# Kernel optimization log

Measured on AMD Instinct MI355X. Metric: run time of the kernel, lower is better.

Reference implementation:

```python
import jax, jax.numpy as jnp
import numpy as np

BEAMS, TEMP, DEPTH, K = 8, 0.4, 3, 3   # beams, router temperature, max_depth, n_experts
EPS, NEG = 1e-5, -1e9

def _conv(x, w, b):
    y = jax.lax.conv_general_dilated(x, w, (1, 1), 'VALID',
                                     dimension_numbers=('NCHW', 'OIHW', 'NCHW'))
    return y + b[None, :, None, None]

def _bn(x, g, b, m, v):
    inv = g * jax.lax.rsqrt(v + EPS)
    return x * inv[None, :, None, None] + (b - m * inv)[None, :, None, None]

def _pool(x):  # AvgPool2d(2)
    return jax.lax.reduce_window(x, 0.0, jax.lax.add, (1, 1, 2, 2), (1, 1, 2, 2), 'VALID') * 0.25

def _fwd(x, conv1_w, conv1_b, bn1_g, bn1_b, bn1_m, bn1_v,
         conv2_w, conv2_b, bn2_g, bn2_b, bn2_m, bn2_v,
         conv3_w, conv3_b, bn3_g, bn3_b, bn3_m, bn3_v,
         Wxh, Whh, bh, Who, bo, emb, Wexp, bexp, Wout, bout):
    B = x.shape[0]
    h = _pool(jax.nn.relu(_bn(_conv(x, conv1_w, conv1_b), bn1_g, bn1_b, bn1_m, bn1_v)))
    h = _pool(jax.nn.relu(_bn(_conv(h, conv2_w, conv2_b), bn2_g, bn2_b, bn2_m, bn2_v)))
    h = _pool(jax.nn.relu(_bn(_conv(h, conv3_w, conv3_b), bn3_g, bn3_b, bn3_m, bn3_v)))
    feat = h.reshape(B, -1)                                  # (B,128)
    # --- beam search over length-3 op sequences with RNN router ---
    hr = jnp.broadcast_to(feat[:, None, :], (B, BEAMS, 128))  # router hidden, (B,beams,128)
    scores = jnp.full((B, BEAMS), NEG, dtype=x.dtype).at[:, 0].set(0.0)
    ops_seq = []
    for _ in range(DEPTH):
        logits = jnp.einsum('bkd,do->bko', hr, Who) + bo      # (B,beams,3)
        logp = jax.nn.log_softmax(logits / TEMP, axis=-1)
        total = (scores[..., None] + logp).reshape(B, BEAMS * K)
        scores, idx = jax.lax.top_k(total, BEAMS)             # (B,beams)
        beam_idx, op = idx // K, idx % K
        hr = jnp.take_along_axis(hr, beam_idx[..., None], axis=1)
        hr = jnp.tanh(hr @ Whh + emb[op] @ Wxh + bh)
        ops_seq = [jnp.take_along_axis(o, beam_idx, axis=1) for o in ops_seq]
        ops_seq.append(op)
    # --- top-1 routed expert chain (grouped gather-GEMM instead of per-sample loop) ---
    hs = jnp.broadcast_to(feat[:, None, :], (B, BEAMS, 128)).reshape(B * BEAMS, 128)
    for op in ops_seq:
        o = op.reshape(B * BEAMS)
        hs = jax.nn.relu(jnp.einsum('nd,ndk->nk', hs, Wexp[o]) + bexp[o])
    return jax.nn.log_softmax(hs @ Wout + bout, axis=1)      # (B*beams,10)

def setup_inputs() -> dict:
    key = jax.random.key(0)
    ks = jax.random.split(key, 20)
    n = lambda i, shape, s: jax.random.normal(ks[i], shape, jnp.float32) * s
    d = {
        'x': jax.random.normal(ks[0], (512, 1, 32, 32), jnp.float32),
        'conv1_w': n(1, (32, 1, 3, 3), 0.2),  'conv1_b': n(2, (32,), 0.02),
        'bn1_g': jnp.ones((32,), jnp.float32), 'bn1_b': jnp.zeros((32,), jnp.float32),
        'bn1_m': jnp.zeros((32,), jnp.float32), 'bn1_v': jnp.ones((32,), jnp.float32),
        'conv2_w': n(3, (32, 32, 3, 3), 0.06), 'conv2_b': n(4, (32,), 0.02),
        'bn2_g': jnp.ones((32,), jnp.float32), 'bn2_b': jnp.zeros((32,), jnp.float32),
        'bn2_m': jnp.zeros((32,), jnp.float32), 'bn2_v': jnp.ones((32,), jnp.float32),
        'conv3_w': n(5, (32, 32, 3, 3), 0.06), 'conv3_b': n(6, (32,), 0.02),
        'bn3_g': jnp.ones((32,), jnp.float32), 'bn3_b': jnp.zeros((32,), jnp.float32),
        'bn3_m': jnp.zeros((32,), jnp.float32), 'bn3_v': jnp.ones((32,), jnp.float32),
        'Wxh': n(7, (128, 128), 0.09), 'Whh': n(8, (128, 128), 0.09), 'bh': n(9, (128,), 0.02),
        'Who': n(10, (128, 3), 0.09), 'bo': n(11, (3,), 0.02), 'emb': n(12, (3, 128), 0.5),
        'Wexp': n(13, (3, 128, 128), 0.09), 'bexp': n(14, (3, 128), 0.02),
        'Wout': n(15, (128, 10), 0.09), 'bout': n(16, (10,), 0.02),
    }
    return d

def reference(x, conv1_w, conv1_b, bn1_g, bn1_b, bn1_m, bn1_v,
              conv2_w, conv2_b, bn2_g, bn2_b, bn2_m, bn2_v,
              conv3_w, conv3_b, bn3_g, bn3_b, bn3_m, bn3_v,
              Wxh, Whh, bh, Who, bo, emb, Wexp, bexp, Wout, bout):
    return _fwd(x, conv1_w, conv1_b, bn1_g, bn1_b, bn1_m, bn1_v,
                conv2_w, conv2_b, bn2_g, bn2_b, bn2_m, bn2_v,
                conv3_w, conv3_b, bn3_g, bn3_b, bn3_m, bn3_v,
                Wxh, Whh, bh, Who, bo, emb, Wexp, bexp, Wout, bout)
```

## Files before the change

### kernel.cpp

```cpp
#include <hip/hip_runtime.h>
#include <math.h>

__global__ __launch_bounds__(512) void conv1_k(
    const float* __restrict__ x, const float* __restrict__ w,
    const float* __restrict__ cb, const float* __restrict__ bg,
    const float* __restrict__ bb, const float* __restrict__ bm,
    const float* __restrict__ bv, float* __restrict__ h1)
{
    __shared__ float img[32 * 33];
    __shared__ float ws_[288];
    __shared__ float scale[32], bias2[32];
    const int b = blockIdx.x, tid = threadIdx.x;
    for (int i = tid; i < 1024; i += 512) {
        const int y = i >> 5, xx = i & 31;
        img[y * 33 + xx] = x[b * 1024 + i];
    }
    if (tid < 288) ws_[tid] = w[tid];
    if (tid < 32) {
        float inv = bg[tid] / sqrtf(bv[tid] + 1e-5f);
        scale[tid] = inv;
        bias2[tid] = (cb[tid] - bm[tid]) * inv + bb[tid];
    }
    __syncthreads();

    const int co = tid >> 4, py = tid & 15;
    if (py < 15) {
        float acc0[30], acc1[30];
        #pragma unroll
        for (int i = 0; i < 30; ++i) { acc0[i] = 0.f; acc1[i] = 0.f; }
        const float* w9 = &ws_[co * 9];
        #pragma unroll
        for (int ir = 0; ir < 4; ++ir) {
            const int y = 2 * py + ir;
            float wk0 = 0.f, wk1 = 0.f, wk2 = 0.f, wl0 = 0.f, wl1 = 0.f, wl2 = 0.f;
            if (ir <= 2) { wk0 = w9[ir * 3 + 0]; wk1 = w9[ir * 3 + 1]; wk2 = w9[ir * 3 + 2]; }
            if (ir >= 1) { wl0 = w9[(ir - 1) * 3 + 0]; wl1 = w9[(ir - 1) * 3 + 1]; wl2 = w9[(ir - 1) * 3 + 2]; }
            #pragma unroll
            for (int xx = 0; xx < 32; ++xx) {
                const float rv = img[y * 33 + xx];
                if (ir <= 2) {
                    if (xx <= 29) acc0[xx] += rv * wk0;
                    if (xx >= 1 && xx <= 30) acc0[xx - 1] += rv * wk1;
                    if (xx >= 2) acc0[xx - 2] += rv * wk2;
                }
                if (ir >= 1) {
                    if (xx <= 29) acc1[xx] += rv * wl0;
                    if (xx >= 1 && xx <= 30) acc1[xx - 1] += rv * wl1;
                    if (xx >= 2) acc1[xx - 2] += rv * wl2;
                }
            }
        }
        const float sc = scale[co], bs = bias2[co];
        #pragma unroll
        for (int px = 0; px < 15; ++px) {
            const float v = fmaxf(acc0[2 * px] * sc + bs, 0.f)
                          + fmaxf(acc0[2 * px + 1] * sc + bs, 0.f)
                          + fmaxf(acc1[2 * px] * sc + bs, 0.f)
                          + fmaxf(acc1[2 * px + 1] * sc + bs, 0.f);
            h1[b * 7200 + co * 225 + py * 15 + px] = v * 0.25f;
        }
    }
}

__global__ __launch_bounds__(384) void conv2_k(
    const float* __restrict__ h1, const float* __restrict__ w,
    const float* __restrict__ cb, const float* __restrict__ bg,
    const float* __restrict__ bb, const float* __restrict__ bm,
    const float* __restrict__ bv, float* __restrict__ h2)
{
    __shared__ float in_s[32 * 210];
    __shared__ float w_s[9216];
    __shared__ float scale[32], bias2[32];
    const int b = blockIdx.x, tid = threadIdx.x;
    for (int i = tid; i < 6720; i += 384) {
        const int ci = i / 210, rem = i % 210;
        in_s[i] = h1[b * 7200 + ci * 225 + rem];
    }
    for (int i = tid; i < 9216; i += 384) {
        const int co = i & 31, k = i >> 5;
        w_s[i] = w[co * 288 + k];
    }
    if (tid < 32) {
        float inv = bg[tid] / sqrtf(bv[tid] + 1e-5f);
        scale[tid] = inv;
        bias2[tid] = (cb[tid] - bm[tid]) * inv + bb[tid];
    }
    __syncthreads();

    const int co = tid & 31, g = tid >> 5;
    const int py = g >> 1, xh = g & 1;
    const int gx0 = xh * 6;
    float acc0[6], acc1[6];
    #pragma unroll
    for (int i = 0; i < 6; ++i) { acc0[i] = 0.f; acc1[i] = 0.f; }

    for (int ci = 0; ci < 32; ++ci) {
        float w9[9];
        #pragma unroll
        for (int kk = 0; kk < 9; ++kk) w9[kk] = w_s[(ci * 9 + kk) * 32 + co];
        const float* ip = &in_s[ci * 210];
        #pragma unroll
        for (int ir = 0; ir < 4; ++ir) {
            const int y = 2 * py + ir;
            const float* rowp = &ip[y * 15 + gx0];
            #pragma unroll
            for (int xx = 0; xx < 8; ++xx) {
                const float rv = rowp[xx];
                if (ir <= 2) {
                    if (xx <= 5) acc0[xx] += rv * w9[ir * 3 + 0];
                    if (xx >= 1 && xx <= 6) acc0[xx - 1] += rv * w9[ir * 3 + 1];
                    if (xx >= 2) acc0[xx - 2] += rv * w9[ir * 3 + 2];
                }
                if (ir >= 1) {
                    if (xx <= 5) acc1[xx] += rv * w9[(ir - 1) * 3 + 0];
                    if (xx >= 1 && xx <= 6) acc1[xx - 1] += rv * w9[(ir - 1) * 3 + 1];
                    if (xx >= 2) acc1[xx - 2] += rv * w9[(ir - 1) * 3 + 2];
                }
            }
        }
    }
    const float sc = scale[co], bs = bias2[co];
    #pragma unroll
    for (int pxl = 0; pxl < 3; ++pxl) {
        const float v = fmaxf(acc0[2 * pxl] * sc + bs, 0.f)
                      + fmaxf(acc0[2 * pxl + 1] * sc + bs, 0.f)
                      + fmaxf(acc1[2 * pxl] * sc + bs, 0.f)
                      + fmaxf(acc1[2 * pxl + 1] * sc + bs, 0.f);
        h2[b * 1152 + co * 36 + py * 6 + xh * 3 + pxl] = v * 0.25f;
    }
}

__global__ __launch_bounds__(128) void conv3_k(
    const float* __restrict__ h2, const float* __restrict__ w,
    const float* __restrict__ cb, const float* __restrict__ bg,
    const float* __restrict__ bb, const float* __restrict__ bm,
    const float* __restrict__ bv, float* __restrict__ feat)
{
    __shared__ float in_s[1152];
    __shared__ float scale[32], bias2[32];
    const int b = blockIdx.x, tid = threadIdx.x;
    for (int i = tid; i < 1152; i += 128) in_s[i] = h2[b * 1152 + i];
    if (tid < 32) {
        float inv = bg[tid] / sqrtf(bv[tid] + 1e-5f);
        scale[tid] = inv;
        bias2[tid] = (cb[tid] - bm[tid]) * inv + bb[tid];
    }
    __syncthreads();
    const int co = tid >> 2, r = tid & 3;
    const int y0 = (r >> 1) * 2, x0 = (r & 1) * 2;
    float s00 = 0.f, s01 = 0.f, s10 = 0.f, s11 = 0.f;
    const float* wco = &w[co * 288];
    for (int ci = 0; ci < 32; ++ci) {
        const float* ip = &in_s[ci * 36 + y0 * 6 + x0];
        float p[4][4];
        for (int i = 0; i < 4; ++i)
            for (int j = 0; j < 4; ++j)
                p[i][j] = ip[i * 6 + j];
        const float* wp = &wco[ci * 9];
        for (int ky = 0; ky < 3; ++ky)
            for (int kx = 0; kx < 3; ++kx) {
                const float wv = wp[ky * 3 + kx];
                s00 += p[ky][kx] * wv;
                s01 += p[ky][kx + 1] * wv;
                s10 += p[ky + 1][kx] * wv;
                s11 += p[ky + 1][kx + 1] * wv;
            }
    }
    const float sc = scale[co], bs = bias2[co];
    float acc = fmaxf(s00 * sc + bs, 0.f) + fmaxf(s01 * sc + bs, 0.f)
              + fmaxf(s10 * sc + bs, 0.f) + fmaxf(s11 * sc + bs, 0.f);
    feat[b * 128 + tid] = acc * 0.25f;
}

__global__ __launch_bounds__(384) void e2_k(
    const float* __restrict__ emb, const float* __restrict__ Wxh,
    const float* __restrict__ bh, float* __restrict__ E2)
{
    const int t = threadIdx.x;
    if (t < 384) {
        const int o = t >> 7, j = t & 127;
        float a = bh[j];
        for (int d = 0; d < 128; ++d) a += emb[o * 128 + d] * Wxh[d * 128 + j];
        E2[t] = a;
    }
}

__global__ __launch_bounds__(256) void router_k(
    const float* __restrict__ feat, const float* __restrict__ Whh,
    const float* __restrict__ Who, const float* __restrict__ bo,
    const float* __restrict__ E2, const float* __restrict__ Wexp,
    const float* __restrict__ bexp, const float* __restrict__ Wout,
    const float* __restrict__ bout, float* __restrict__ out)
{
    const int b = blockIdx.x, tid = threadIdx.x;
    __shared__ float fs[128];
    __shared__ float hbuf[2][8][128];
    __shared__ float E2s[384];
    __shared__ float total[24];
    __shared__ float scores[8];
    __shared__ int bi[8];
    __shared__ int opsel[8];
    __shared__ int oph[3][8];
    __shared__ int oph2[3][8];
    __shared__ float l10[8][10];
    __shared__ float lsebuf[8];

    if (tid < 128) fs[tid] = feat[b * 128 + tid];
    for (int i = tid; i < 384; i += 256) E2s[i] = E2[i];
    if (tid < 8) scores[tid] = (tid == 0) ? 0.f : -1.0e9f;
    __syncthreads();
    {
        float* h0 = &hbuf[0][0][0];
        for (int i = tid; i < 1024; i += 256) h0[i] = fs[i & 127];
    }
    __syncthreads();

    int cur = 0;
    for (int t = 0; t < 3; ++t) {
        {
            const int g = tid >> 5, l = tid & 31;
            float p0 = 0.f, p1 = 0.f, p2 = 0.f;
            for (int d = l; d < 128; d += 32) {
                const float h = hbuf[cur][g][d];
                p0 += h * Who[d * 3 + 0];
                p1 += h * Who[d * 3 + 1];
                p2 += h * Who[d * 3 + 2];
            }
            for (int s = 16; s > 0; s >>= 1) {
                p0 += __shfl_down(p0, s, 32);
                p1 += __shfl_down(p1, s, 32);
                p2 += __shfl_down(p2, s, 32);
            }
            if (l == 0) {
                const float t0 = (p0 + bo[0]) / 0.4f;
                const float t1 = (p1 + bo[1]) / 0.4f;
                const float t2 = (p2 + bo[2]) / 0.4f;
                const float mm = fmaxf(t0, fmaxf(t1, t2));
                const float lse = mm + logf(expf(t0 - mm) + expf(t1 - mm) + expf(t2 - mm));
                const float sc = scores[g];
                total[g * 3 + 0] = sc + (t0 - lse);
                total[g * 3 + 1] = sc + (t1 - lse);
                total[g * 3 + 2] = sc + (t2 - lse);
            }
        }
        __syncthreads();
        if (tid == 0) {
            for (int r = 0; r < 8; ++r) {
                float best = -INFINITY; int idx = 0;
                for (int i = 0; i < 24; ++i) {
                    const float vv = total[i];
                    if (vv > best) { best = vv; idx = i; }
                }
                total[idx] = -INFINITY;
                scores[r] = best;
                bi[r] = idx / 3;
                opsel[r] = idx % 3;
            }
            for (int r = 0; r < 8; ++r) {
                for (int s = 0; s < t; ++s) oph2[s][r] = oph[s][bi[r]];
                oph2[t][r] = opsel[r];
            }
            for (int r = 0; r < 8; ++r)
                for (int s = 0; s <= t; ++s) oph[s][r] = oph2[s][r];
        }
        __syncthreads();
        {
            const int j = tid & 127, half = tid >> 7;
            const int n0 = half, n1 = half + 2, n2 = half + 4, n3 = half + 6;
            float a0 = E2s[opsel[n0] * 128 + j];
            float a1 = E2s[opsel[n1] * 128 + j];
            float a2 = E2s[opsel[n2] * 128 + j];
            float a3 = E2s[opsel[n3] * 128 + j];
            const float* r0 = hbuf[cur][bi[n0]];
            const float* r1 = hbuf[cur][bi[n1]];
            const float* r2 = hbuf[cur][bi[n2]];
            const float* r3 = hbuf[cur][bi[n3]];
            for (int d = 0; d < 128; ++d) {
                const float wv = Whh[d * 128 + j];
                a0 += r0[d] * wv;
                a1 += r1[d] * wv;
                a2 += r2[d] * wv;
                a3 += r3[d] * wv;
            }
            const int nxt = cur ^ 1;
            hbuf[nxt][n0][j] = tanhf(a0);
            hbuf[nxt][n1][j] = tanhf(a1);
            hbuf[nxt][n2][j] = tanhf(a2);
            hbuf[nxt][n3][j] = tanhf(a3);
        }
        cur ^= 1;
        __syncthreads();
    }

    {
        float* h0 = &hbuf[0][0][0];
        for (int i = tid; i < 1024; i += 256) h0[i] = fs[i & 127];
    }
    __syncthreads();
    int c2 = 0;
    for (int t = 0; t < 3; ++t) {
        const int j = tid & 127, half = tid >> 7;
        const int n0 = half, n1 = half + 2, n2 = half + 4, n3 = half + 6;
        const int o0 = oph[t][n0], o1 = oph[t][n1], o2 = oph[t][n2], o3 = oph[t][n3];
        float a0 = bexp[o0 * 128 + j];
        float a1 = bexp[o1 * 128 + j];
        float a2 = bexp[o2 * 128 + j];
        float a3 = bexp[o3 * 128 + j];
        const float* r0 = hbuf[c2][n0];
        const float* r1 = hbuf[c2][n1];
        const float* r2 = hbuf[c2][n2];
        const float* r3 = hbuf[c2][n3];
        const float* w0 = &Wexp[o0 * 16384 + j];
        const float* w1 = &Wexp[o1 * 16384 + j];
        const float* w2 = &Wexp[o2 * 16384 + j];
        const float* w3 = &Wexp[o3 * 16384 + j];
        for (int d = 0; d < 128; ++d) {
            a0 += r0[d] * w0[d * 128];
            a1 += r1[d] * w1[d * 128];
            a2 += r2[d] * w2[d * 128];
            a3 += r3[d] * w3[d * 128];
        }
        const int nxt = c2 ^ 1;
        hbuf[nxt][n0][j] = fmaxf(a0, 0.f);
        hbuf[nxt][n1][j] = fmaxf(a1, 0.f);
        hbuf[nxt][n2][j] = fmaxf(a2, 0.f);
        hbuf[nxt][n3][j] = fmaxf(a3, 0.f);
        c2 ^= 1;
        __syncthreads();
    }

    if (tid < 80) {
        const int nb = tid / 10, c = tid % 10;
        float acc = bout[c];
        const float* hrow = hbuf[c2][nb];
        for (int d = 0; d < 128; ++d) acc += hrow[d] * Wout[d * 10 + c];
        l10[nb][c] = acc;
    }
    __syncthreads();
    if (tid < 8) {
        float mm = l10[tid][0];
        for (int c = 1; c < 10; ++c) mm = fmaxf(mm, l10[tid][c]);
        float s = 0.f;
        for (int c = 0; c < 10; ++c) s += expf(l10[tid][c] - mm);
        lsebuf[tid] = mm + logf(s);
    }
    __syncthreads();
    if (tid < 80) {
        const int nb = tid / 10, c = tid % 10;
        out[(b * 8 + nb) * 10 + c] = l10[nb][c] - lsebuf[nb];
    }
}

extern "C" void kernel_launch(void* const* d_in, const int* in_sizes, int n_in,
                              void* d_out, int out_size, void* d_ws, size_t ws_size,
                              hipStream_t stream) {
    (void)in_sizes; (void)n_in; (void)out_size; (void)ws_size;
    const float* x    = (const float*)d_in[0];
    const float* c1w  = (const float*)d_in[1];
    const float* c1b  = (const float*)d_in[2];
    const float* g1   = (const float*)d_in[3];
    const float* b1   = (const float*)d_in[4];
    const float* m1   = (const float*)d_in[5];
    const float* v1   = (const float*)d_in[6];
    const float* c2w  = (const float*)d_in[7];
    const float* c2b  = (const float*)d_in[8];
    const float* g2   = (const float*)d_in[9];
    const float* b2   = (const float*)d_in[10];
    const float* m2   = (const float*)d_in[11];
    const float* v2   = (const float*)d_in[12];
    const float* c3w  = (const float*)d_in[13];
    const float* c3b  = (const float*)d_in[14];
    const float* g3   = (const float*)d_in[15];
    const float* b3   = (const float*)d_in[16];
    const float* m3   = (const float*)d_in[17];
    const float* v3   = (const float*)d_in[18];
    const float* Wxh  = (const float*)d_in[19];
    const float* Whh  = (const float*)d_in[20];
    const float* bh   = (const float*)d_in[21];
    const float* Who  = (const float*)d_in[22];
    const float* bo   = (const float*)d_in[23];
    const float* emb  = (const float*)d_in[24];
    const float* Wexp = (const float*)d_in[25];
    const float* bexp = (const float*)d_in[26];
    const float* Wout = (const float*)d_in[27];
    const float* bout = (const float*)d_in[28];

    float* ws   = (float*)d_ws;
    float* h1   = ws;
    float* h2   = h1 + 3686400;
    float* feat = h2 + 589824;
    float* E2   = feat + 65536;

    e2_k<<<1, 384, 0, stream>>>(emb, Wxh, bh, E2);
    conv1_k<<<512, 512, 0, stream>>>(x, c1w, c1b, g1, b1, m1, v1, h1);
    conv2_k<<<512, 384, 0, stream>>>(h1, c2w, c2b, g2, b2, m2, v2, h2);
    conv3_k<<<512, 128, 0, stream>>>(h2, c3w, c3b, g3, b3, m3, v3, feat);
    router_k<<<512, 256, 0, stream>>>(feat, Whh, Who, bo, E2, Wexp, bexp, Wout, bout,
                                      (float*)d_out);
}
```

Baseline: 246.9 us.

## Restructure conv3 and router kernels: split-K conv3, fold E2 into router, vectorize GEMVs

conv3 now uses 256 threads, stages transposed weights in shared memory and splits the input channels into two halves that are summed through shared memory. The separate E2 kernel is removed and each router block recomputes the embedding projection itself, which saves one launch but repeats that work in every block. The router and expert GEMVs are remapped to one wavefront per beam, each lane holding four outputs loaded as float4, and the final log-softmax uses wave shuffles instead of shared memory and barriers. Top-k selection keeps values in registers with a bitmask, and several barriers are removed.

```diff
diff --git a/kernel.cpp b/kernel.cpp
--- a/kernel.cpp
+++ b/kernel.cpp
@@ -130,102 +130,120 @@
     }
 }
 
-__global__ __launch_bounds__(128) void conv3_k(
+__global__ __launch_bounds__(256) void conv3_k(
     const float* __restrict__ h2, const float* __restrict__ w,
     const float* __restrict__ cb, const float* __restrict__ bg,
     const float* __restrict__ bb, const float* __restrict__ bm,
     const float* __restrict__ bv, float* __restrict__ feat)
 {
     __shared__ float in_s[1152];
+    __shared__ float w_s[9216];
+    __shared__ float psum[2][4][4][33];
     __shared__ float scale[32], bias2[32];
     const int b = blockIdx.x, tid = threadIdx.x;
-    for (int i = tid; i < 1152; i += 128) in_s[i] = h2[b * 1152 + i];
+    for (int i = tid; i < 1152; i += 256) in_s[i] = h2[b * 1152 + i];
+    for (int i = tid; i < 9216; i += 256) {
+        const int co = i & 31, k = i >> 5;
+        w_s[i] = w[co * 288 + k];
+    }
     if (tid < 32) {
         float inv = bg[tid] / sqrtf(bv[tid] + 1e-5f);
         scale[tid] = inv;
         bias2[tid] = (cb[tid] - bm[tid]) * inv + bb[tid];
     }
     __syncthreads();
-    const int co = tid >> 2, r = tid & 3;
-    const int y0 = (r >> 1) * 2, x0 = (r & 1) * 2;
+
+    const int co = tid & 31, g = tid >> 5;
+    const int pos = g & 3, h = g >> 2;
+    const int y0 = (pos >> 1) * 2, x0 = (pos & 1) * 2;
     float s00 = 0.f, s01 = 0.f, s10 = 0.f, s11 = 0.f;
-    const float* wco = &w[co * 288];
-    for (int ci = 0; ci < 32; ++ci) {
+    for (int ci = h * 16; ci < h * 16 + 16; ++ci) {
+        float w9[9];
+        #pragma unroll
+        for (int kk = 0; kk < 9; ++kk) w9[kk] = w_s[(ci * 9 + kk) * 32 + co];
         const float* ip = &in_s[ci * 36 + y0 * 6 + x0];
         float p[4][4];
+        #pragma unroll
         for (int i = 0; i < 4; ++i)
+            #pragma unroll
             for (int j = 0; j < 4; ++j)
                 p[i][j] = ip[i * 6 + j];
-        const float* wp = &wco[ci * 9];
+        #pragma unroll
         for (int ky = 0; ky < 3; ++ky)
+            #pragma unroll
             for (int kx = 0; kx < 3; ++kx) {
-                const float wv = wp[ky * 3 + kx];
+                const float wv = w9[ky * 3 + kx];
                 s00 += p[ky][kx] * wv;
                 s01 += p[ky][kx + 1] * wv;
                 s10 += p[ky + 1][kx] * wv;
                 s11 += p[ky + 1][kx + 1] * wv;
             }
     }
-    const float sc = scale[co], bs = bias2[co];
-    float acc = fmaxf(s00 * sc + bs, 0.f) + fmaxf(s01 * sc + bs, 0.f)
-              + fmaxf(s10 * sc + bs, 0.f) + fmaxf(s11 * sc + bs, 0.f);
-    feat[b * 128 + tid] = acc * 0.25f;
-}
-
-__global__ __launch_bounds__(384) void e2_k(
-    const float* __restrict__ emb, const float* __restrict__ Wxh,
-    const float* __restrict__ bh, float* __restrict__ E2)
-{
-    const int t = threadIdx.x;
-    if (t < 384) {
-        const int o = t >> 7, j = t & 127;
-        float a = bh[j];
-        for (int d = 0; d < 128; ++d) a += emb[o * 128 + d] * Wxh[d * 128 + j];
-        E2[t] = a;
+    psum[h][pos][0][co] = s00;
+    psum[h][pos][1][co] = s01;
+    psum[h][pos][2][co] = s10;
+    psum[h][pos][3][co] = s11;
+    __syncthreads();
+    if (h == 0) {
+        const float sc = scale[co], bs = bias2[co];
+        float v = 0.f;
+        #pragma unroll
+        for (int k = 0; k < 4; ++k) {
+            const float sk = psum[0][pos][k][co] + psum[1][pos][k][co];
+            v += fmaxf(sk * sc + bs, 0.f);
+        }
+        feat[b * 128 + co * 4 + pos] = v * 0.25f;
     }
 }
 
 __global__ __launch_bounds__(256) void router_k(
     const float* __restrict__ feat, const float* __restrict__ Whh,
     const float* __restrict__ Who, const float* __restrict__ bo,
-    const float* __restrict__ E2, const float* __restrict__ Wexp,
+    const float* __restrict__ emb, const float* __restrict__ Wxh,
+    const float* __restrict__ bh, const float* __restrict__ Wexp,
     const float* __restrict__ bexp, const float* __restrict__ Wout,
     const float* __restrict__ bout, float* __restrict__ out)
 {
     const int b = blockIdx.x, tid = threadIdx.x;
-    __shared__ float fs[128];
-    __shared__ float hbuf[2][8][128];
-    __shared__ float E2s[384];
+    const int g = tid >> 5, l = tid & 31, j0 = l * 4;
+    __shared__ __align__(16) float fs[128];
+    __shared__ __align__(16) float hbuf[2][8][128];
+    __shared__ __align__(16) float E2s[3][128];
     __shared__ float total[24];
     __shared__ float scores[8];
     __shared__ int bi[8];
     __shared__ int opsel[8];
     __shared__ int oph[3][8];
     __shared__ int oph2[3][8];
-    __shared__ float l10[8][10];
-    __shared__ float lsebuf[8];
 
     if (tid < 128) fs[tid] = feat[b * 128 + tid];
-    for (int i = tid; i < 384; i += 256) E2s[i] = E2[i];
-    if (tid < 8) scores[tid] = (tid == 0) ? 0.f : -1.0e9f;
+    for (int i = tid; i < 384; i += 256) {
+        const int o = i >> 7, j = i & 127;
+        float a = bh[j];
+        #pragma unroll 4
+        for (int d = 0; d < 128; ++d) a += emb[o * 128 + d] * Wxh[d * 128 + j];
+        E2s[o][j] = a;
+    }
+    if (l == 0) scores[g] = (g == 0) ? 0.f : -1.0e9f;
     __syncthreads();
     {
-        float* h0 = &hbuf[0][0][0];
-        for (int i = tid; i < 1024; i += 256) h0[i] = fs[i & 127];
-    }
-    __syncthreads();
+        const float4 f4 = *reinterpret_cast<const float4*>(&fs[j0]);
+        *reinterpret_cast<float4*>(&hbuf[0][g][j0]) = f4;
+    }
 
     int cur = 0;
     for (int t = 0; t < 3; ++t) {
         {
-            const int g = tid >> 5, l = tid & 31;
             float p0 = 0.f, p1 = 0.f, p2 = 0.f;
-            for (int d = l; d < 128; d += 32) {
-                const float h = hbuf[cur][g][d];
-                p0 += h * Who[d * 3 + 0];
-                p1 += h * Who[d * 3 + 1];
-                p2 += h * Who[d * 3 + 2];
-            }
+            #pragma unroll
+            for (int dd = 0; dd < 4; ++dd) {
+                const int d = l + 32 * dd;
+                const float hv = hbuf[cur][g][d];
+                p0 += hv * Who[d * 3 + 0];
+                p1 += hv * Who[d * 3 + 1];
+                p2 += hv * Who[d * 3 + 2];
+            }
+            #pragma unroll
             for (int s = 16; s > 0; s >>= 1) {
                 p0 += __shfl_down(p0, s, 32);
                 p1 += __shfl_down(p1, s, 32);
@@ -245,13 +263,17 @@
         }
         __syncthreads();
         if (tid == 0) {
+            float tv[24];
+            #pragma unroll
+            for (int i = 0; i < 24; ++i) tv[i] = total[i];
+            unsigned mask = 0;
             for (int r = 0; r < 8; ++r) {
                 float best = -INFINITY; int idx = 0;
+                #pragma unroll
                 for (int i = 0; i < 24; ++i) {
-                    const float vv = total[i];
-                    if (vv > best) { best = vv; idx = i; }
-                }
-                total[idx] = -INFINITY;
+                    if (!(mask & (1u << i)) && tv[i] > best) { best = tv[i]; idx = i; }
+                }
+                mask |= 1u << idx;
                 scores[r] = best;
                 bi[r] = idx / 3;
                 opsel[r] = idx % 3;
@@ -265,89 +287,65 @@
         }
         __syncthreads();
         {
-            const int j = tid & 127, half = tid >> 7;
-            const int n0 = half, n1 = half + 2, n2 = half + 4, n3 = half + 6;
-            float a0 = E2s[opsel[n0] * 128 + j];
-            float a1 = E2s[opsel[n1] * 128 + j];
-            float a2 = E2s[opsel[n2] * 128 + j];
-            float a3 = E2s[opsel[n3] * 128 + j];
-            const float* r0 = hbuf[cur][bi[n0]];
-            const float* r1 = hbuf[cur][bi[n1]];
-            const float* r2 = hbuf[cur][bi[n2]];
-            const float* r3 = hbuf[cur][bi[n3]];
+            const int o = opsel[g], src = bi[g];
+            float4 a = *reinterpret_cast<const float4*>(&E2s[o][j0]);
+            const float* hrow = &hbuf[cur][src][0];
+            #pragma unroll 4
             for (int d = 0; d < 128; ++d) {
-                const float wv = Whh[d * 128 + j];
-                a0 += r0[d] * wv;
-                a1 += r1[d] * wv;
-                a2 += r2[d] * wv;
-                a3 += r3[d] * wv;
-            }
+                const float rv = hrow[d];
+                const float4 w4 = *reinterpret_cast<const float4*>(&Whh[d * 128 + j0]);
+                a.x += rv * w4.x; a.y += rv * w4.y; a.z += rv * w4.z; a.w += rv * w4.w;
+            }
+            float4 tr;
+            tr.x = tanhf(a.x); tr.y = tanhf(a.y); tr.z = tanhf(a.z); tr.w = tanhf(a.w);
             const int nxt = cur ^ 1;
-            hbuf[nxt][n0][j] = tanhf(a0);
-            hbuf[nxt][n1][j] = tanhf(a1);
-            hbuf[nxt][n2][j] = tanhf(a2);
-            hbuf[nxt][n3][j] = tanhf(a3);
+            *reinterpret_cast<float4*>(&hbuf[nxt][g][j0]) = tr;
         }
         cur ^= 1;
         __syncthreads();
     }
 
     {
-        float* h0 = &hbuf[0][0][0];
-        for (int i = tid; i < 1024; i += 256) h0[i] = fs[i & 127];
-    }
-    __syncthreads();
+        const float4 f4 = *reinterpret_cast<const float4*>(&fs[j0]);
+        *reinterpret_cast<float4*>(&hbuf[0][g][j0]) = f4;
+    }
     int c2 = 0;
     for (int t = 0; t < 3; ++t) {
-        const int j = tid & 127, half = tid >> 7;
-        const int n0 = half, n1 = half + 2, n2 = half + 4, n3 = half + 6;
-        const int o0 = oph[t][n0], o1 = oph[t][n1], o2 = oph[t][n2], o3 = oph[t][n3];
-        float a0 = bexp[o0 * 128 + j];
-        float a1 = bexp[o1 * 128 + j];
-        float a2 = bexp[o2 * 128 + j];
-        float a3 = bexp[o3 * 128 + j];
-        const float* r0 = hbuf[c2][n0];
-        const float* r1 = hbuf[c2][n1];
-        const float* r2 = hbuf[c2][n2];
-        const float* r3 = hbuf[c2][n3];
-        const float* w0 = &Wexp[o0 * 16384 + j];
-        const float* w1 = &Wexp[o1 * 16384 + j];
-        const float* w2 = &Wexp[o2 * 16384 + j];
-        const float* w3 = &Wexp[o3 * 16384 + j];
+        const int o = oph[t][g];
+        const float* wbase = &Wexp[o * 16384];
+        float4 a = *reinterpret_cast<const float4*>(&bexp[o * 128 + j0]);
+        const float* hrow = &hbuf[c2][g][0];
+        #pragma unroll 4
         for (int d = 0; d < 128; ++d) {
-            a0 += r0[d] * w0[d * 128];
-            a1 += r1[d] * w1[d * 128];
-            a2 += r2[d] * w2[d * 128];
-            a3 += r3[d] * w3[d * 128];
-        }
+            const float rv = hrow[d];
+            const float4 w4 = *reinterpret_cast<const float4*>(&wbase[d * 128 + j0]);
+            a.x += rv * w4.x; a.y += rv * w4.y; a.z += rv * w4.z; a.w += rv * w4.w;
+        }
+        float4 rr;
+        rr.x = fmaxf(a.x, 0.f); rr.y = fmaxf(a.y, 0.f);
+        rr.z = fmaxf(a.z, 0.f); rr.w = fmaxf(a.w, 0.f);
         const int nxt = c2 ^ 1;
-        hbuf[nxt][n0][j] = fmaxf(a0, 0.f);
-        hbuf[nxt][n1][j] = fmaxf(a1, 0.f);
-        hbuf[nxt][n2][j] = fmaxf(a2, 0.f);
-        hbuf[nxt][n3][j] = fmaxf(a3, 0.f);
+        *reinterpret_cast<float4*>(&hbuf[nxt][g][j0]) = rr;
         c2 ^= 1;
-        __syncthreads();
-    }
-
-    if (tid < 80) {
-        const int nb = tid / 10, c = tid % 10;
-        float acc = bout[c];
-        const float* hrow = hbuf[c2][nb];
-        for (int d = 0; d < 128; ++d) acc += hrow[d] * Wout[d * 10 + c];
-        l10[nb][c] = acc;
-    }
-    __syncthreads();
-    if (tid < 8) {
-        float mm = l10[tid][0];
-        for (int c = 1; c < 10; ++c) mm = fmaxf(mm, l10[tid][c]);
-        float s = 0.f;
-        for (int c = 0; c < 10; ++c) s += expf(l10[tid][c] - mm);
-        lsebuf[tid] = mm + logf(s);
-    }
-    __syncthreads();
-    if (tid < 80) {
-        const int nb = tid / 10, c = tid % 10;
-        out[(b * 8 + nb) * 10 + c] = l10[nb][c] - lsebuf[nb];
+    }
+
+    {
+        float acc = 0.f;
+        if (l < 10) {
+            acc = bout[l];
+            const float* hrow = &hbuf[c2][g][0];
+            #pragma unroll 4
+            for (int d = 0; d < 128; ++d) acc += hrow[d] * Wout[d * 10 + l];
+        }
+        float mm = (l < 10) ? acc : -INFINITY;
+        #pragma unroll
+        for (int s = 16; s > 0; s >>= 1) mm = fmaxf(mm, __shfl_xor(mm, s, 32));
+        float ex = (l < 10) ? expf(acc - mm) : 0.f;
+        float sum = ex;
+        #pragma unroll
+        for (int s = 16; s > 0; s >>= 1) sum += __shfl_xor(sum, s, 32);
+        const float lse = mm + logf(sum);
+        if (l < 10) out[(b * 8 + g) * 10 + l] = acc - lse;
     }
 }
 
@@ -389,12 +387,10 @@
     float* h1   = ws;
     float* h2   = h1 + 3686400;
     float* feat = h2 + 589824;
-    float* E2   = feat + 65536;
-
-    e2_k<<<1, 384, 0, stream>>>(emb, Wxh, bh, E2);
+
     conv1_k<<<512, 512, 0, stream>>>(x, c1w, c1b, g1, b1, m1, v1, h1);
     conv2_k<<<512, 384, 0, stream>>>(h1, c2w, c2b, g2, b2, m2, v2, h2);
-    conv3_k<<<512, 128, 0, stream>>>(h2, c3w, c3b, g3, b3, m3, v3, feat);
-    router_k<<<512, 256, 0, stream>>>(feat, Whh, Who, bo, E2, Wexp, bexp, Wout, bout,
-                                      (float*)d_out);
-}
+    conv3_k<<<512, 256, 0, stream>>>(h2, c3w, c3b, g3, b3, m3, v3, feat);
+    router_k<<<512, 256, 0, stream>>>(feat, Whh, Who, bo, emb, Wxh, bh,
+                                      Wexp, bexp, Wout, bout, (float*)d_out);
+}
```

Measured after the change: 275.3 us. 11.5% more time.
